# Performance work log

Hardware: AMD Instinct MI355X
Metric: run time of the kernel (lower is better)

The kernel has to match this reference:

```python
import jax, jax.numpy as jnp
import numpy as np

HID = 512; HH = HID // 2; INP = 1; OUT = 1
INH = int(HID * 0.3); EXC = HID - INH            # 153 / 359
N = 3 * HH + 2 * HID + INP                       # 1793 total units
ALM_EXC_START = 3 * HH + HID                      # start of ALM excitatory block
T_CONST = 0.1; SIGMA_REC = 0.01
B, T = 128, 300


def _np_masks():
    rng = np.random.default_rng(0)
    n_zeros = int(np.ceil(0.9 * HH))
    sparse = np.ones((HH, HH), np.float32)
    for c in range(HH):
        sparse[rng.permutation(HH)[:n_zeros], c] = 0.0
    alm2str = np.concatenate([np.ones((HH, EXC), np.float32), np.zeros((HH, INH), np.float32)], 1)
    thal2d1 = np.concatenate([np.ones((HH // 2, HID), np.float32), np.zeros((HH // 2, HID), np.float32)], 0)
    alm2d1 = 1.0 - thal2d1
    iti2d1 = np.concatenate([np.ones((HH // 2, INP), np.float32), np.zeros((HH // 2, INP), np.float32)], 0)
    alm_sign = np.concatenate([np.ones(EXC, np.float32), -np.ones(INH, np.float32)])  # alm2alm_D diagonal
    return sparse, alm2str, thal2d1, alm2d1, iti2d1, alm_sign

_SPARSE, _ALM2STR, _THAL2D1M, _ALM2D1M, _ITI2D1M, _ALMSIGN = [jnp.asarray(a) for a in _np_masks()]


def _clip(w):
    return jnp.clip(w, 1e-10, 1.0)               # F.hardtanh(w, 1e-10, 1)


def _build_W(d12d1_w, d12d2_w, d22d1_w, d22d2_w, d22stn_w, d12thal_w, stn2thal_w,
             thal2alm_w, alm2alm_w, thal2d1_w, thal2d2_w, alm2d1_w, alm2d2_w,
             inp_w_d1, inp_w_d2):
    z_ss = jnp.zeros((HH, HH)); z_sl = jnp.zeros((HH, HID))
    z_ls = jnp.zeros((HID, HH)); z_ll = jnp.zeros((HID, HID))
    z_si = jnp.zeros((HH, INP)); z_li = jnp.zeros((HID, INP))
    # striatal recurrence: sparse_mask * hardtanh(w) @ (-I)
    d12d1 = -(_SPARSE * _clip(d12d1_w)); d12d2 = -(_SPARSE * _clip(d12d2_w))
    d22d1 = -(_SPARSE * _clip(d22d1_w)); d22d2 = -(_SPARSE * _clip(d22d2_w))
    row_d1 = jnp.concatenate([d12d1, d22d1, z_ss, _THAL2D1M * _clip(thal2d1_w),
                              _ALM2D1M * _ALM2STR * _clip(alm2d1_w), _ITI2D1M * _clip(inp_w_d1)], 1)
    row_d2 = jnp.concatenate([d12d2, d22d2, z_ss, _clip(thal2d2_w),
                              _ALM2STR * _clip(alm2d2_w), _clip(inp_w_d2)], 1)
    row_stn = jnp.concatenate([z_ss, _clip(d22stn_w), z_ss, z_sl, z_sl, z_si], 1)
    row_thal = jnp.concatenate([_clip(d12thal_w), z_ls, -_clip(stn2thal_w), z_ll, z_ll, z_li], 1)  # stn2thal @ (-I)
    row_alm = jnp.concatenate([z_ls, z_ls, z_ls, _clip(thal2alm_w),
                               _clip(alm2alm_w) * _ALMSIGN[None, :], z_li], 1)      # alm2alm @ D (Dale)
    row_iti = jnp.zeros((INP, N))
    return jnp.concatenate([row_d1, row_d2, row_stn, row_thal, row_alm, row_iti], 0)


def setup_inputs() -> dict:
    key = jax.random.key(0)
    ks = jax.random.split(key, 24)
    u = lambda k, s: jax.random.uniform(k, s, jnp.float32) * 0.01   # uniform(0, 0.01) init
    return {
        "inp": jax.random.uniform(ks[0], (B, T, INP), jnp.float32),
        "cue_inp": jax.random.uniform(ks[1], (B, T, INP), jnp.float32),
        "inhib_stim": jnp.zeros((B, T, N), jnp.float32),
        "hn": jax.random.uniform(ks[2], (1, B, N), jnp.float32),
        "xn": jax.random.uniform(ks[3], (1, B, N), jnp.float32),
        "noise": jax.random.normal(ks[4], (B, T, N), jnp.float32),
        "d12d1_w": u(ks[5], (HH, HH)), "d12d2_w": u(ks[6], (HH, HH)),
        "d22d1_w": u(ks[7], (HH, HH)), "d22d2_w": u(ks[8], (HH, HH)),
        "d22stn_w": u(ks[9], (HH, HH)), "d12thal_w": u(ks[10], (HID, HH)),
        "stn2thal_w": u(ks[11], (HID, HH)), "thal2alm_w": u(ks[12], (HID, HID)),
        "alm2alm_w": u(ks[13], (HID, HID)), "thal2d1_w": u(ks[14], (HH, HID)),
        "thal2d2_w": u(ks[15], (HH, HID)), "alm2d1_w": u(ks[16], (HH, HID)),
        "alm2d2_w": u(ks[17], (HH, HID)), "inp_w_d1": u(ks[18], (HH, INP)),
        "inp_w_d2": u(ks[19], (HH, INP)), "out_w_alm": u(ks[20], (OUT, EXC)),
    }


def reference(inp, cue_inp, inhib_stim, hn, xn, noise,
              d12d1_w, d12d2_w, d22d1_w, d22d2_w, d22stn_w, d12thal_w, stn2thal_w,
              thal2alm_w, alm2alm_w, thal2d1_w, thal2d2_w, alm2d1_w, alm2d2_w,
              inp_w_d1, inp_w_d2, out_w_alm):
    W = _build_W(d12d1_w, d12d2_w, d22d1_w, d22d2_w, d22stn_w, d12thal_w, stn2thal_w,
                 thal2alm_w, alm2alm_w, thal2d1_w, thal2d2_w, alm2d1_w, alm2d2_w,
                 inp_w_d1, inp_w_d2)
    # tonic current: 0.1 everywhere except ITI units
    tonic = jnp.concatenate([0.1 * jnp.ones(N - INP, jnp.float32), jnp.zeros(INP, jnp.float32)])
    seq = (inhib_stim.swapaxes(0, 1),                 # [T, B, N]
           (inp + cue_inp).swapaxes(0, 1),            # [T, B, INP] -> injected into ITI units
           noise.swapaxes(0, 1))                      # [T, B, N]

    def step(carry, s):
        x, h = carry
        inh_t, iti_t, noise_t = s
        drive = h @ W.T + tonic + inh_t + SIGMA_REC * noise_t
        drive = drive.at[:, N - INP:].add(iti_t)
        x = x + T_CONST * (-x + drive)
        h = jax.nn.relu(x)
        out = h[:, ALM_EXC_START:ALM_EXC_START + EXC] @ out_w_alm.T
        return (x, h), (h, x, out)

    (_, _), (hs, xs, outs) = jax.lax.scan(step, (xn[0], hn[0]), seq)
    return hs.swapaxes(0, 1), xs.swapaxes(0, 1), outs.swapaxes(0, 1)
```

## Files before the change

### kernel.cpp

```cpp
#include <hip/hip_runtime.h>
#include <stdint.h>
#include <string.h>

#define NREAL 1793
#define NPAD  1824
#define NROWP 1808
#define WSTR  1832
#define NBLK  113
#define NGRP  2
#define TSTEPS 300
#define BATCH 128
#define XS_OFF 68851200
#define OUT_OFF 137702400
#define LOFF (16 * WSTR)
#define LOSCALE 4096.0f
#define LOINV  2.44140625e-4f

#define ARR_IDX(g,s)  (((g) * 8 + (s)) * 32)
#define MID_IDX(g)    ((16 + (g)) * 32)
#define FLAG_IDX(g,s) ((18 + (g) * 8 + (s)) * 32)
#define STRIPE_SZ(s)  ((s) == 0 ? 15u : 14u)

typedef _Float16 half_t;
typedef __attribute__((ext_vector_type(8))) _Float16 half8;
typedef __attribute__((ext_vector_type(4))) float f32x4;
typedef __attribute__((ext_vector_type(4))) unsigned int uint4v;

__device__ __forceinline__ float clipw(float w) {
  return fminf(fmaxf(w, 1e-10f), 1.0f);
}

__device__ __forceinline__ void store_pack_llc(uint32_t* p, uint32_t v) {
  asm volatile("global_store_dword %0, %1, off sc0 sc1"
               :: "v"((unsigned long long)(uintptr_t)p), "v"(v)
               : "memory");
}

__device__ __forceinline__ float unpack_h(uint32_t p) {
  unsigned short uh = (unsigned short)(p & 0xffffu);
  unsigned short ul = (unsigned short)(p >> 16);
  half_t hh = *(half_t*)&uh;
  half_t hl = *(half_t*)&ul;
  return (float)hh + LOINV * (float)hl;
}

template<int LO0, int N0, int LO1, int N1, int LO2, int N2>
__device__ __forceinline__ void seg_mfma(const uint32_t* __restrict__ ap,
                                         const half_t* __restrict__ Wl, int wl_b,
                                         f32x4& acc0, f32x4& acc1, f32x4& acc2)
{
  constexpr int NC = N0 + N1 + N2;
  if (NC == 0) return;
  uint4v q0[NC ? NC : 1], q1[NC ? NC : 1];
  #pragma unroll
  for (int i = 0; i < NC; ++i) {
    const int kc = (i < N0) ? (LO0 + i)
                 : (i < N0 + N1) ? (LO1 + i - N0)
                 : (LO2 + i - N0 - N1);
    q0[i] = *(const uint4v*)(ap + kc * 32);
    q1[i] = *(const uint4v*)(ap + kc * 32 + 4);
  }
  #pragma unroll
  for (int i = 0; i < NC; ++i) {
    const int kc = (i < N0) ? (LO0 + i)
                 : (i < N0 + N1) ? (LO1 + i - N0)
                 : (LO2 + i - N0 - N1);
    uint4v uh, ul;
    uh.x = __builtin_amdgcn_perm(q0[i].y, q0[i].x, 0x05040100u);
    uh.y = __builtin_amdgcn_perm(q0[i].w, q0[i].z, 0x05040100u);
    uh.z = __builtin_amdgcn_perm(q1[i].y, q1[i].x, 0x05040100u);
    uh.w = __builtin_amdgcn_perm(q1[i].w, q1[i].z, 0x05040100u);
    ul.x = __builtin_amdgcn_perm(q0[i].y, q0[i].x, 0x07060302u);
    ul.y = __builtin_amdgcn_perm(q0[i].w, q0[i].z, 0x07060302u);
    ul.z = __builtin_amdgcn_perm(q1[i].y, q1[i].x, 0x07060302u);
    ul.w = __builtin_amdgcn_perm(q1[i].w, q1[i].z, 0x07060302u);
    union { uint4v u; half8 h; } ch, cl;
    ch.u = uh; cl.u = ul;
    half8 bvh = *(const half8*)&Wl[wl_b + kc * 32];
    half8 bvl = *(const half8*)&Wl[LOFF + wl_b + kc * 32];
    acc0 = __builtin_amdgcn_mfma_f32_16x16x32_f16(ch.h, bvh, acc0, 0, 0, 0);
    acc1 = __builtin_amdgcn_mfma_f32_16x16x32_f16(ch.h, bvl, acc1, 0, 0, 0);
    acc2 = __builtin_amdgcn_mfma_f32_16x16x32_f16(cl.h, bvh, acc2, 0, 0, 0);
  }
}

__global__ __launch_bounds__(256)
void build_w(const float* __restrict__ d12d1, const float* __restrict__ d12d2,
             const float* __restrict__ d22d1, const float* __restrict__ d22d2,
             const float* __restrict__ d22stn, const float* __restrict__ d12thal,
             const float* __restrict__ stn2thal, const float* __restrict__ thal2alm,
             const float* __restrict__ alm2alm, const float* __restrict__ thal2d1,
             const float* __restrict__ thal2d2, const float* __restrict__ alm2d1,
             const float* __restrict__ alm2d2, const float* __restrict__ inpw1,
             const float* __restrict__ inpw2, const unsigned int* __restrict__ mbits,
             half_t* __restrict__ W)
{
  int idx = blockIdx.x * 256 + threadIdx.x;
  if (idx >= NROWP * NPAD) return;
  int i = idx / NPAD, j = idx - (idx / NPAD) * NPAD;
  float v = 0.f;
  if (i < NREAL && j < NREAL) {
    if (i < 256) {
      if (j < 512) {
        int jj = j & 255;
        unsigned bit = (mbits[(i << 3) + (jj >> 5)] >> (jj & 31)) & 1u;
        float wv = (j < 256) ? d12d1[(i << 8) + jj] : d22d1[(i << 8) + jj];
        v = bit ? -clipw(wv) : 0.f;
      } else if (j < 768) {
      } else if (j < 1280) {
        if (i < 128) v = clipw(thal2d1[(i << 9) + (j - 768)]);
      } else if (j < 1792) {
        int jj = j - 1280;
        if (i >= 128 && jj < 359) v = clipw(alm2d1[(i << 9) + jj]);
      } else {
        if (i < 128) v = clipw(inpw1[i]);
      }
    } else if (i < 512) {
      int ii = i - 256;
      if (j < 512) {
        int jj = j & 255;
        unsigned bit = (mbits[(ii << 3) + (jj >> 5)] >> (jj & 31)) & 1u;
        float wv = (j < 256) ? d12d2[(ii << 8) + jj] : d22d2[(ii << 8) + jj];
        v = bit ? -clipw(wv) : 0.f;
      } else if (j < 768) {
      } else if (j < 1280) {
        v = clipw(thal2d2[(ii << 9) + (j - 768)]);
      } else if (j < 1792) {
        int jj = j - 1280;
        if (jj < 359) v = clipw(alm2d2[(ii << 9) + jj]);
      } else {
        v = clipw(inpw2[ii]);
      }
    } else if (i < 768) {
      int ii = i - 512;
      if (j >= 256 && j < 512) v = clipw(d22stn[(ii << 8) + (j - 256)]);
    } else if (i < 1280) {
      int ii = i - 768;
      if (j < 256) v = clipw(d12thal[(ii << 8) + j]);
      else if (j >= 512 && j < 768) v = -clipw(stn2thal[(ii << 8) + (j - 512)]);
    } else if (i < 1792) {
      int ii = i - 1280;
      if (j >= 768 && j < 1280) v = clipw(thal2alm[(ii << 9) + (j - 768)]);
      else if (j >= 1280) {
        int jj = j - 1280;
        v = clipw(alm2alm[(ii << 9) + jj]) * ((jj < 359) ? 1.f : -1.f);
      }
    }
  }
  half_t vh = (half_t)v;
  half_t vl = (half_t)((v - (float)vh) * LOSCALE);
  W[idx] = vh;
  W[(size_t)NROWP * NPAD + idx] = vl;
}

__global__ __launch_bounds__(256)
void init_h(const float* __restrict__ hn, uint32_t* __restrict__ hbuf)
{
  const size_t P4 = (size_t)BATCH * NPAD;
  int idx = blockIdx.x * 256 + threadIdx.x;
  if (idx >= BATCH * NPAD) return;
  int b = idx / NPAD, k = idx - b * NPAD;
  float v = (k < NREAL) ? hn[b * NREAL + k] : 0.f;
  half_t vh = (half_t)v;
  half_t vl = (half_t)((v - (float)vh) * LOSCALE);
  uint32_t hp = (uint32_t)(*(unsigned short*)&vh) |
                ((uint32_t)(*(unsigned short*)&vl) << 16);
  hbuf[idx]      = hp;
  hbuf[P4 + idx] = 0u;
}

__global__ __launch_bounds__(256, 1)
void rnn_step_all(const half_t* __restrict__ Wg, uint32_t* __restrict__ hbuf,
                  unsigned int* __restrict__ cnt,
                  const float* __restrict__ inp, const float* __restrict__ cue,
                  const float* __restrict__ inhib, const float* __restrict__ noise,
                  const float* __restrict__ xn, const float* __restrict__ outw,
                  float* __restrict__ dout)
{
  __shared__ __align__(16) half_t Wl[2 * 16 * WSTR];
  const int tid = threadIdx.x;
  const int bid = blockIdx.x;
  const int g  = bid / NBLK;
  const int nb = bid - g * NBLK;
  const int r0 = nb * 16;
  const int bg = g * 64;
  const size_t P4 = (size_t)BATCH * NPAD;

  const int lane = tid & 63;
  const int w    = tid >> 6;
  const int n_i  = lane & 15;
  const int kq   = lane >> 4;
  const int row  = r0 + n_i;
  const bool valid = row < NREAL;
  const int b0 = bg + 16 * w + kq * 4;
  const int bA = bg + 16 * w + n_i;
  const int wl_b = n_i * WSTR + kq * 8;
  const bool is_outblk = (r0 == 512);

  float inh[4], noi[4];
  #pragma unroll
  for (int r = 0; r < 4; ++r) {
    inh[r] = 0.f; noi[r] = 0.f;
    if (valid) {
      int ei = ((b0 + r) * TSTEPS) * NREAL + row;
      inh[r] = __builtin_nontemporal_load(&inhib[ei]);
      noi[r] = __builtin_nontemporal_load(&noise[ei]);
    }
  }

  for (int idx = tid; idx < 2 * 16 * (NPAD / 8); idx += 256) {
    int p   = idx / (16 * (NPAD / 8));
    int rem = idx - p * 16 * (NPAD / 8);
    int rr  = rem / (NPAD / 8);
    int cc  = (rem - rr * (NPAD / 8)) * 8;
    *(uint4v*)&Wl[p * LOFF + rr * WSTR + cc] =
        *(const uint4v*)&Wg[(size_t)p * NROWP * NPAD + (size_t)(r0 + rr) * NPAD + cc];
  }
  __syncthreads();

  float xr[4];
  #pragma unroll
  for (int r = 0; r < 4; ++r)
    xr[r] = valid ? xn[(size_t)(b0 + r) * NREAL + row] : 0.f;

  const float tonic = (valid && row < 1792) ? 0.1f : 0.f;
  const bool is_iti = (row == 1792);

  const int ob    = bg + 16 * w + (lane >> 2);
  const int opart = lane & 3;
  const int ou0   = opart * 90;
  const int onu   = (opart == 3) ? 89 : 90;

  #pragma unroll 1
  for (int t = 0; t < TSTEPS; ++t) {
    const uint32_t* hr = hbuf + (size_t)(t & 1) * P4;
    uint32_t*       hw = hbuf + (size_t)((t & 1) ^ 1) * P4;

    float itv[4];
    #pragma unroll
    for (int r = 0; r < 4; ++r) {
      int bt = (b0 + r) * TSTEPS + t;
      itv[r] = is_iti ? (inp[bt] + cue[bt]) : 0.f;
    }

    const uint32_t* ap = hr + (size_t)bA * NPAD + kq * 8;
    f32x4 acc0 = {0.f, 0.f, 0.f, 0.f};
    f32x4 acc1 = {0.f, 0.f, 0.f, 0.f};
    f32x4 acc2 = {0.f, 0.f, 0.f, 0.f};

    if      (r0 < 128)  seg_mfma<0, 16, 24, 16, 56, 1>(ap, Wl, wl_b, acc0, acc1, acc2);
    else if (r0 < 256)  seg_mfma<0, 16, 40, 12,  0, 0>(ap, Wl, wl_b, acc0, acc1, acc2);
    else if (r0 < 512)  seg_mfma<0, 16, 24, 28, 56, 1>(ap, Wl, wl_b, acc0, acc1, acc2);
    else if (r0 < 768)  seg_mfma<8,  8,  0,  0,  0, 0>(ap, Wl, wl_b, acc0, acc1, acc2);
    else if (r0 < 1280) seg_mfma<0,  8, 16,  8,  0, 0>(ap, Wl, wl_b, acc0, acc1, acc2);
    else if (r0 < 1792) seg_mfma<24, 32, 0,  0,  0, 0>(ap, Wl, wl_b, acc0, acc1, acc2);

    #pragma unroll
    for (int r = 0; r < 4; ++r) {
      float drive = acc0[r] + LOINV * (acc1[r] + acc2[r])
                    + tonic + inh[r] + 0.01f * noi[r] + itv[r];
      float xv = xr[r] + 0.1f * (drive - xr[r]);
      float hv = fmaxf(xv, 0.f);
      xr[r] = xv;
      int bt = (b0 + r) * TSTEPS + t;
      if (valid) {
        int ei = bt * NREAL + row;
        __builtin_nontemporal_store(hv, &dout[ei]);
        __builtin_nontemporal_store(xv, &dout[XS_OFF + ei]);
      }
      half_t hh = (half_t)hv;
      half_t hl = (half_t)((hv - (float)hh) * LOSCALE);
      uint32_t hp = (uint32_t)(*(unsigned short*)&hh) |
                    ((uint32_t)(*(unsigned short*)&hl) << 16);
      store_pack_llc(&hw[(size_t)(b0 + r) * NPAD + row], hp);
    }

    if (is_outblk && t >= 1) {
      const uint32_t* hb = hr + (size_t)ob * NPAD + 1280 + ou0;
      float s = 0.f;
      #pragma unroll 10
      for (int i = 0; i < onu; ++i)
        s += unpack_h(hb[i]) * outw[ou0 + i];
      s += __shfl_xor(s, 1);
      s += __shfl_xor(s, 2);
      if (opart == 0)
        __builtin_nontemporal_store(s, &dout[OUT_OFF + ob * TSTEPS + (t - 1)]);
    }

    if (t + 1 < TSTEPS) {
      #pragma unroll
      for (int r = 0; r < 4; ++r) {
        if (valid) {
          int ei = ((b0 + r) * TSTEPS + (t + 1)) * NREAL + row;
          inh[r] = __builtin_nontemporal_load(&inhib[ei]);
          noi[r] = __builtin_nontemporal_load(&noise[ei]);
        }
      }
      asm volatile("s_waitcnt vmcnt(8)" ::: "memory");
      __builtin_amdgcn_s_barrier();
      if (tid == 0) {
        const int s = nb & 7;
        const unsigned epoch = (unsigned)(t + 1);
        unsigned old = atomicAdd(&cnt[ARR_IDX(g, s)], 1u);
        if (old == epoch * STRIPE_SZ(s) - 1u) {
          unsigned mo = atomicAdd(&cnt[MID_IDX(g)], 1u);
          if (mo == epoch * 8u - 1u) {
            #pragma unroll
            for (int f = 0; f < 8; ++f)
              __hip_atomic_store(&cnt[FLAG_IDX(g, f)], epoch,
                                 __ATOMIC_RELAXED, __HIP_MEMORY_SCOPE_AGENT);
          }
        }
        int spins = 0;
        while (__hip_atomic_load(&cnt[FLAG_IDX(g, s)], __ATOMIC_RELAXED,
                                 __HIP_MEMORY_SCOPE_AGENT) < epoch) {
          if (spins < 4) {
            __builtin_amdgcn_s_sleep(1);
          } else {
            __builtin_amdgcn_s_sleep(8);
          }
          ++spins;
        }
        __builtin_amdgcn_fence(__ATOMIC_ACQUIRE, "agent");
      }
      __builtin_amdgcn_s_barrier();
    }
  }

  asm volatile("s_waitcnt vmcnt(0)" ::: "memory");
  __builtin_amdgcn_s_barrier();
  if (tid == 0) {
    const int s = nb & 7;
    const unsigned epoch = (unsigned)TSTEPS;
    unsigned old = atomicAdd(&cnt[ARR_IDX(g, s)], 1u);
    if (old == epoch * STRIPE_SZ(s) - 1u) {
      unsigned mo = atomicAdd(&cnt[MID_IDX(g)], 1u);
      if (mo == epoch * 8u - 1u) {
        #pragma unroll
        for (int f = 0; f < 8; ++f)
          __hip_atomic_store(&cnt[FLAG_IDX(g, f)], epoch,
                             __ATOMIC_RELAXED, __HIP_MEMORY_SCOPE_AGENT);
      }
    }
  }
  if (is_outblk) {
    if (tid == 0) {
      const int s = nb & 7;
      int spins = 0;
      while (__hip_atomic_load(&cnt[FLAG_IDX(g, s)], __ATOMIC_RELAXED,
                               __HIP_MEMORY_SCOPE_AGENT) < (unsigned)TSTEPS) {
        if (spins < 4) {
          __builtin_amdgcn_s_sleep(1);
        } else {
          __builtin_amdgcn_s_sleep(8);
        }
        ++spins;
      }
      __builtin_amdgcn_fence(__ATOMIC_ACQUIRE, "agent");
    }
    __builtin_amdgcn_s_barrier();
    const uint32_t* hr = hbuf + (size_t)(TSTEPS & 1) * P4;
    const uint32_t* hb = hr + (size_t)ob * NPAD + 1280 + ou0;
    float s = 0.f;
    #pragma unroll 10
    for (int i = 0; i < onu; ++i)
      s += unpack_h(hb[i]) * outw[ou0 + i];
    s += __shfl_xor(s, 1);
    s += __shfl_xor(s, 2);
    if (opart == 0)
      __builtin_nontemporal_store(s, &dout[OUT_OFF + ob * TSTEPS + (TSTEPS - 1)]);
  }
}

static void compute_sparse_mask(uint32_t* mb) {
  uint32_t pool[4];
  uint32_t hc = 0x43b0d7e5u;
  auto hashmix = [&hc](uint32_t value) -> uint32_t {
    value ^= hc; hc *= 0x931e8875u; value *= hc; value ^= value >> 16; return value;
  };
  auto mixf = [](uint32_t x, uint32_t y) -> uint32_t {
    uint32_t r = x * 0xca01f9ddu;
    r -= y * 0x4973f715u;
    r ^= r >> 16;
    return r;
  };
  for (int i = 0; i < 4; ++i) pool[i] = hashmix(0u);
  for (int s = 0; s < 4; ++s)
    for (int d = 0; d < 4; ++d)
      if (s != d) pool[d] = mixf(pool[d], hashmix(pool[s]));
  uint32_t st[8];
  uint32_t hb = 0x8b51f9ddu;
  for (int i = 0; i < 8; ++i) {
    uint32_t dv = pool[i & 3];
    dv ^= hb; hb *= 0x58f38dedu; dv *= hb; dv ^= dv >> 16;
    st[i] = dv;
  }
  uint64_t v64[4];
  for (int i = 0; i < 4; ++i) v64[i] = (uint64_t)st[2 * i] | ((uint64_t)st[2 * i + 1] << 32);
  typedef unsigned __int128 u128;
  const u128 MULT = ((u128)0x2360ed051fc65da4ULL << 64) | 0x4385df649fccf645ULL;
  u128 initstate = ((u128)v64[0] << 64) | v64[1];
  u128 initseq   = ((u128)v64[2] << 64) | v64[3];
  u128 state = 0, inc = (initseq << 1) | 1;
  state = state * MULT + inc;
  state += initstate;
  state = state * MULT + inc;
  bool has32 = false; uint32_t cached = 0;
  auto next64 = [&]() -> uint64_t {
    state = state * MULT + inc;
    uint64_t hi = (uint64_t)(state >> 64), lo = (uint64_t)state;
    unsigned rot = (unsigned)(state >> 122);
    uint64_t x = hi ^ lo;
    return (x >> rot) | (x << ((64 - rot) & 63));
  };
  auto next32 = [&]() -> uint32_t {
    if (has32) { has32 = false; return cached; }
    uint64_t v = next64();
    has32 = true; cached = (uint32_t)(v >> 32);
    return (uint32_t)v;
  };
  auto rinterval = [&](uint32_t mx) -> uint32_t {
    if (mx == 0) return 0;
    uint32_t mask = mx;
    mask |= mask >> 1; mask |= mask >> 2; mask |= mask >> 4;
    mask |= mask >> 8; mask |= mask >> 16;
    uint32_t value;
    do { value = next32() & mask; } while (value > mx);
    return value;
  };
  for (int i = 0; i < 256 * 8; ++i) mb[i] = 0xFFFFFFFFu;
  int perm[256];
  for (int c = 0; c < 256; ++c) {
    for (int i = 0; i < 256; ++i) perm[i] = i;
    for (int i = 255; i >= 1; --i) {
      uint32_t j = rinterval((uint32_t)i);
      int tmp = perm[i]; perm[i] = perm[j]; perm[j] = tmp;
    }
    for (int z = 0; z < 231; ++z)
      mb[perm[z] * 8 + (c >> 5)] &= ~(1u << (c & 31));
  }
}

extern "C" void kernel_launch(void* const* d_in, const int* in_sizes, int n_in,
                              void* d_out, int out_size, void* d_ws, size_t ws_size,
                              hipStream_t stream)
{
  (void)in_sizes; (void)n_in; (void)out_size; (void)ws_size;
  const float* inp   = (const float*)d_in[0];
  const float* cue   = (const float*)d_in[1];
  const float* inhib = (const float*)d_in[2];
  const float* hn    = (const float*)d_in[3];
  const float* xn    = (const float*)d_in[4];
  const float* noise = (const float*)d_in[5];
  const float* outw  = (const float*)d_in[21];
  float* dout = (float*)d_out;

  char* ws = (char*)d_ws;
  const size_t W_BYTES = (size_t)2 * NROWP * NPAD * sizeof(half_t);
  const size_t H_BYTES = (size_t)2 * BATCH * NPAD * 4;
  half_t*   W    = (half_t*)ws;
  uint32_t* hbuf = (uint32_t*)(ws + W_BYTES);
  unsigned int* mbits = (unsigned int*)(ws + W_BYTES + H_BYTES);
  unsigned int* cnt   = (unsigned int*)(ws + W_BYTES + H_BYTES + 8192);

  static uint32_t hmask[256 * 8];
  compute_sparse_mask(hmask);
  (void)hipMemcpyAsync(mbits, hmask, sizeof(hmask), hipMemcpyHostToDevice, stream);
  (void)hipMemsetAsync(cnt, 0, 8192, stream);

  build_w<<<(NROWP * NPAD + 255) / 256, 256, 0, stream>>>(
      (const float*)d_in[6],  (const float*)d_in[7],  (const float*)d_in[8],
      (const float*)d_in[9],  (const float*)d_in[10], (const float*)d_in[11],
      (const float*)d_in[12], (const float*)d_in[13], (const float*)d_in[14],
      (const float*)d_in[15], (const float*)d_in[16], (const float*)d_in[17],
      (const float*)d_in[18], (const float*)d_in[19], (const float*)d_in[20],
      mbits, W);
  init_h<<<(BATCH * NPAD + 255) / 256, 256, 0, stream>>>(hn, hbuf);

  void* args[] = {(void*)&W, (void*)&hbuf, (void*)&cnt, (void*)&inp, (void*)&cue,
                  (void*)&inhib, (void*)&noise, (void*)&xn, (void*)&outw, (void*)&dout};
  hipError_t err = hipLaunchCooperativeKernel(reinterpret_cast<void*>(rnn_step_all),
                                              dim3(NGRP * NBLK), dim3(256), args, 0, stream);
  if (err != hipSuccess) {
    rnn_step_all<<<dim3(NGRP * NBLK), dim3(256), 0, stream>>>(
        W, hbuf, cnt, inp, cue, inhib, noise, xn, outw, dout);
  }
}
```

Before: 4.177 ms.

## Use per-XCC leader to poll grid barrier flag and rebroadcast locally

Each XCD (found by reading the XCC_ID hardware register) elects one leader block per group, preferring lightly loaded blocks. Only the leader spins on the global stripe flag, then republishes the epoch to a per-XCC flag; the other blocks poll that flag and invalidate their L2-side caches with buffer_inv sc0 instead of taking a full agent acquire fence. The aim is to cut contention on the global flag and the cost of the acquire in the per-timestep barrier. Output stores also change from nontemporal to sc0 sc1 stores. The scheme adds a second hop of latency and relies on buffer_inv sc0 being enough for coherence.

New measurement: 4.133 ms. About the same (-1.0%).

```diff
diff --git a/kernel.cpp b/kernel.cpp
--- a/kernel.cpp
+++ b/kernel.cpp
@@ -19,6 +19,8 @@
 #define ARR_IDX(g,s)  (((g) * 8 + (s)) * 32)
 #define MID_IDX(g)    ((16 + (g)) * 32)
 #define FLAG_IDX(g,s) ((18 + (g) * 8 + (s)) * 32)
+#define XLDR_IDX(g,x) ((40 + (g) * 8 + (x)) * 32)
+#define XFLG_IDX(g,x) ((56 + (g) * 8 + (x)) * 32)
 #define STRIPE_SZ(s)  ((s) == 0 ? 15u : 14u)
 
 typedef _Float16 half_t;
@@ -31,6 +33,11 @@
 }
 
 __device__ __forceinline__ void store_pack_llc(uint32_t* p, uint32_t v) {
+  asm volatile("global_store_dword %0, %1, off sc0 sc1"
+               :: "v"((unsigned long long)(uintptr_t)p), "v"(v)
+               : "memory");
+}
+__device__ __forceinline__ void store_f32_llc(float* p, float v) {
   asm volatile("global_store_dword %0, %1, off sc0 sc1"
                :: "v"((unsigned long long)(uintptr_t)p), "v"(v)
                : "memory");
@@ -196,6 +203,16 @@
   const int bA = bg + 16 * w + n_i;
   const int wl_b = n_i * WSTR + kq * 8;
   const bool is_outblk = (r0 == 512);
+  const bool light = (r0 >= 512 && r0 < 1280) || (r0 == 1792);
+
+  uint32_t xcc = 0;
+  bool isldr = false;
+  if (tid == 0) {
+    asm volatile("s_getreg_b32 %0, hwreg(HW_REG_XCC_ID)" : "=s"(xcc));
+    xcc &= 7u;
+    if (light)
+      isldr = (atomicCAS(&cnt[XLDR_IDX(g, xcc)], 0u, (uint32_t)bid + 1u) == 0u);
+  }
 
   float inh[4], noi[4];
   #pragma unroll
@@ -217,6 +234,12 @@
         *(const uint4v*)&Wg[(size_t)p * NROWP * NPAD + (size_t)(r0 + rr) * NPAD + cc];
   }
   __syncthreads();
+
+  if (tid == 0 && !light) {
+    if (__hip_atomic_load(&cnt[XLDR_IDX(g, xcc)], __ATOMIC_RELAXED,
+                          __HIP_MEMORY_SCOPE_AGENT) == 0u)
+      isldr = (atomicCAS(&cnt[XLDR_IDX(g, xcc)], 0u, (uint32_t)bid + 1u) == 0u);
+  }
 
   float xr[4];
   #pragma unroll
@@ -265,8 +288,8 @@
       int bt = (b0 + r) * TSTEPS + t;
       if (valid) {
         int ei = bt * NREAL + row;
-        __builtin_nontemporal_store(hv, &dout[ei]);
-        __builtin_nontemporal_store(xv, &dout[XS_OFF + ei]);
+        store_f32_llc(&dout[ei], hv);
+        store_f32_llc(&dout[XS_OFF + ei], xv);
       }
       half_t hh = (half_t)hv;
       half_t hl = (half_t)((hv - (float)hh) * LOSCALE);
@@ -311,17 +334,28 @@
                                  __ATOMIC_RELAXED, __HIP_MEMORY_SCOPE_AGENT);
           }
         }
-        int spins = 0;
-        while (__hip_atomic_load(&cnt[FLAG_IDX(g, s)], __ATOMIC_RELAXED,
-                                 __HIP_MEMORY_SCOPE_AGENT) < epoch) {
-          if (spins < 4) {
-            __builtin_amdgcn_s_sleep(1);
-          } else {
-            __builtin_amdgcn_s_sleep(8);
+        if (isldr) {
+          int spins = 0;
+          while (__hip_atomic_load(&cnt[FLAG_IDX(g, s)], __ATOMIC_RELAXED,
+                                   __HIP_MEMORY_SCOPE_AGENT) < epoch) {
+            if (spins < 4) { __builtin_amdgcn_s_sleep(1); }
+            else           { __builtin_amdgcn_s_sleep(8); }
+            ++spins;
           }
-          ++spins;
+          __builtin_amdgcn_fence(__ATOMIC_ACQUIRE, "agent");
+          asm volatile("s_waitcnt vmcnt(0)" ::: "memory");
+          __hip_atomic_store(&cnt[XFLG_IDX(g, xcc)], epoch,
+                             __ATOMIC_RELAXED, __HIP_MEMORY_SCOPE_AGENT);
+        } else {
+          int spins = 0;
+          while (__hip_atomic_load(&cnt[XFLG_IDX(g, xcc)], __ATOMIC_RELAXED,
+                                   __HIP_MEMORY_SCOPE_AGENT) < epoch) {
+            if (spins < 4) { __builtin_amdgcn_s_sleep(1); }
+            else           { __builtin_amdgcn_s_sleep(8); }
+            ++spins;
+          }
+          asm volatile("buffer_inv sc0" ::: "memory");
         }
-        __builtin_amdgcn_fence(__ATOMIC_ACQUIRE, "agent");
       }
       __builtin_amdgcn_s_barrier();
     }
@@ -349,11 +383,8 @@
       int spins = 0;
       while (__hip_atomic_load(&cnt[FLAG_IDX(g, s)], __ATOMIC_RELAXED,
                                __HIP_MEMORY_SCOPE_AGENT) < (unsigned)TSTEPS) {
-        if (spins < 4) {
-          __builtin_amdgcn_s_sleep(1);
-        } else {
-          __builtin_amdgcn_s_sleep(8);
-        }
+        if (spins < 4) { __builtin_amdgcn_s_sleep(1); }
+        else           { __builtin_amdgcn_s_sleep(8); }
         ++spins;
       }
       __builtin_amdgcn_fence(__ATOMIC_ACQUIRE, "agent");
@@ -461,12 +492,12 @@
   half_t*   W    = (half_t*)ws;
   uint32_t* hbuf = (uint32_t*)(ws + W_BYTES);
   unsigned int* mbits = (unsigned int*)(ws + W_BYTES + H_BYTES);
-  unsigned int* cnt   = (unsigned int*)(ws + W_BYTES + H_BYTES + 8192);
+  unsigned int* cnt   = (unsigned int*)(ws + W_BYTES + H_BYTES + 16384);
 
   static uint32_t hmask[256 * 8];
   compute_sparse_mask(hmask);
   (void)hipMemcpyAsync(mbits, hmask, sizeof(hmask), hipMemcpyHostToDevice, stream);
-  (void)hipMemsetAsync(cnt, 0, 8192, stream);
+  (void)hipMemsetAsync(cnt, 0, 16384, stream);
 
   build_w<<<(NROWP * NPAD + 255) / 256, 256, 0, stream>>>(
       (const float*)d_in[6],  (const float*)d_in[7],  (const float*)d_in[8],
```
